# Performance work log

Hardware: AMD Instinct MI355X
Metric: run time of the kernel (lower is better)

## Reference

```python
import jax, jax.numpy as jnp
import numpy as np

B, S, D = 16, 4096, 64
N_HASHES, BUCKET_SIZE = 8, 64
TOKEN_SELF_ATTN_VALUE = -50000.0


def setup_inputs() -> dict:
    key = jax.random.key(0)
    k1, k2, k3 = jax.random.split(key, 3)
    qk = jax.random.normal(k1, (B, S, D), jnp.float32)
    v = jax.random.normal(k2, (B, S, D), jnp.float32)
    # random rotations for LSH hashing: (batch, dim, n_hashes, n_buckets//2)
    rotations = jax.random.normal(k3, (B, D, N_HASHES, (S // BUCKET_SIZE) // 2), jnp.float32)
    return {"qk": qk, "v": v, "rotations": rotations}


def _look_one_back(x):
    # concat each chunk with the previous chunk (wrapping): (b, c, n, ...) -> (b, c, 2n, ...)
    return jnp.concatenate([x, jnp.roll(x, 1, axis=1)], axis=2)


def _lsh_attention(qk, v, rotations):
    b, s, d = qk.shape
    n_buckets = s // BUCKET_SIZE
    # --- hash vectors (rehash_each_round=True path) ---
    rotated = jnp.einsum('btf,bfhi->bhti', qk, rotations)          # (b, h, s, nb/2)
    rotated = jnp.concatenate([rotated, -rotated], axis=-1)        # (b, h, s, nb)
    buckets = jnp.argmax(rotated, axis=-1)                          # (b, h, s)
    offsets = (jnp.arange(N_HASHES) * n_buckets)[None, :, None]
    buckets = (buckets + offsets).reshape(b, -1)                    # (b, h*s)
    # --- stable bucket sort of tokens ---
    ticker = jnp.arange(N_HASHES * s)[None, :]
    buckets_and_t = s * buckets + ticker % s
    sticker = jnp.argsort(buckets_and_t, axis=-1)                   # sorted order
    undo_sort = jnp.argsort(sticker, axis=-1)
    st = sticker % s                                                # original token index
    sqk = jnp.take_along_axis(qk, st[..., None], axis=1)            # (b, h*s, d)
    sv = jnp.take_along_axis(v, st[..., None], axis=1)
    chunk_size = N_HASHES * n_buckets
    bq_t = st.reshape(b, chunk_size, -1)                            # (b, c, n)
    bqk = sqk.reshape(b, chunk_size, -1, d)                         # (b, c, n, d)
    bv = sv.reshape(b, chunk_size, -1, d)
    # shared-QK: keys are L2-normalized queries
    norm = jnp.linalg.norm(bqk, axis=-1, keepdims=True)
    bk = bqk / jnp.maximum(norm, 1e-12)
    bk = _look_one_back(bk)                                         # (b, c, 2n, d)
    bvl = _look_one_back(bv)
    bkv_t = _look_one_back(bq_t)                                    # (b, c, 2n)
    dots = jnp.einsum('bhie,bhje->bhij', bqk, bk) * (d ** -0.5)     # (b, c, n, 2n)
    # mask self-attention (token attends to itself only as last resort)
    self_mask = bq_t[:, :, :, None] == bkv_t[:, :, None, :]
    dots = jnp.where(self_mask, TOKEN_SELF_ATTN_VALUE, dots)
    # stable softmax per chunk; keep logsumexp for cross-round combination
    lse = jax.nn.logsumexp(dots, axis=-1, keepdims=True)            # (b, c, n, 1)
    p = jnp.exp(dots - lse)
    bo = jnp.einsum('buij,buje->buie', p, bvl)                      # (b, c, n, d)
    so = bo.reshape(b, -1, d)                                       # (b, h*s, d)
    slogits = lse.reshape(b, -1)                                    # (b, h*s)
    # undo the sort
    o = jnp.take_along_axis(so, undo_sort[..., None], axis=1)
    logits = jnp.take_along_axis(slogits, undo_sort, axis=1)
    o = o.reshape(b, N_HASHES, s, d)
    logits = logits.reshape(b, N_HASHES, s, 1)
    # combine hash rounds weighted by softmax over per-round logsumexp
    probs = jnp.exp(logits - jax.nn.logsumexp(logits, axis=1, keepdims=True))
    return jnp.sum(o * probs, axis=1)                               # (b, s, d)


def reference(qk, v, rotations):
    return _lsh_attention(qk, v, rotations)
```

## Files before the change

kernel.cpp:

```cpp
#include <hip/hip_runtime.h>
#include <math.h>

#define NB_B 16
#define NB_S 4096
#define NB_D 64
#define NB_H 8

#define KSTR 72
#define PSTR 136
#define VSTR 72

typedef _Float16 half_t;
typedef __attribute__((ext_vector_type(2))) _Float16 half2t;
typedef __attribute__((ext_vector_type(4))) _Float16 half4;
typedef __attribute__((ext_vector_type(8))) _Float16 half8;
typedef __attribute__((ext_vector_type(4))) float floatx4;
typedef __attribute__((ext_vector_type(2))) float f32x2;

__global__ __launch_bounds__(256) void prep_kernel(const float* __restrict__ qk,
                                                   const float* __restrict__ v,
                                                   half_t* __restrict__ khat,
                                                   half_t* __restrict__ vh,
                                                   float* __restrict__ norm) {
  int g = blockIdx.x * 256 + threadIdx.x;
  float4 qv = ((const float4*)qk)[g];
  float4 vv = ((const float4*)v)[g];
  float ss = qv.x * qv.x + qv.y * qv.y + qv.z * qv.z + qv.w * qv.w;
  for (int off = 1; off < 16; off <<= 1) ss += __shfl_xor(ss, off);
  float nr = fmaxf(sqrtf(ss), 1e-12f);
  float sc = 1.0f / nr;
  half4 hk = {(half_t)(qv.x * sc), (half_t)(qv.y * sc), (half_t)(qv.z * sc),
              (half_t)(qv.w * sc)};
  half4 hv = {(half_t)vv.x, (half_t)vv.y, (half_t)vv.z, (half_t)vv.w};
  ((half4*)khat)[g] = hk;
  ((half4*)vh)[g] = hv;
  if ((threadIdx.x & 15) == 0) norm[g >> 4] = nr;
}

__global__ __launch_bounds__(256) void hash_kernel(const float* __restrict__ qk,
                                                   const float* __restrict__ rot,
                                                   int* __restrict__ bkt) {
  __shared__ float rotS[64 * 32];
  int tid = threadIdx.x;
  int blk = blockIdx.x;
  int tile = blk & 15, bh = blk >> 4;
  int h = bh & 7, b = bh >> 3;
  int t = (tile << 8) + tid;

  for (int i = tid; i < 2048; i += 256) {
    int f = i >> 5, ii = i & 31;
    rotS[i] = rot[(((size_t)b * 64 + f) * 8 + h) * 32 + ii];
  }
  __syncthreads();

  const float4* qrow = (const float4*)(qk + (((size_t)b << 12) + t) * 64);
  float qreg[64];
#pragma unroll
  for (int j = 0; j < 16; j++) *(float4*)(qreg + 4 * j) = qrow[j];

  f32x2 acc2[16];
#pragma unroll
  for (int i = 0; i < 16; i++) acc2[i] = (f32x2){0.f, 0.f};

  {
#pragma clang fp contract(off)
#pragma unroll
    for (int f = 0; f < 64; f++) {
      float qf = qreg[f];
      f32x2 q2 = {qf, qf};
      const f32x2* wrow = (const f32x2*)(rotS + f * 32);
#pragma unroll
      for (int i2 = 0; i2 < 16; i2++) {
        f32x2 prod = q2 * wrow[i2];
        acc2[i2] = acc2[i2] + prod;
      }
    }
  }

  float b1 = acc2[0][0];
  int i1 = 0;
#pragma unroll
  for (int i = 1; i < 32; i++) {
    float x = acc2[i >> 1][i & 1];
    if (x > b1) { b1 = x; i1 = i; }
  }
#pragma unroll
  for (int i = 0; i < 32; i++) {
    float x = -acc2[i >> 1][i & 1];
    if (x > b1) { b1 = x; i1 = 32 + i; }
  }
  bkt[(((size_t)(b * 8 + h)) << 12) + t] = i1;
}

__global__ __launch_bounds__(256) void sort_kernel(const int* __restrict__ bkt,
                                                   int* __restrict__ st) {
  __shared__ int lb[4096];
  __shared__ int hist[4096];
  __shared__ int cumoff[64];
  int tid = threadIdx.x;
  int b = blockIdx.x >> 3, h = blockIdx.x & 7;
  const int* gb = bkt + (((size_t)(b * 8 + h)) << 12);
  for (int t = tid; t < 4096; t += 256) lb[t] = gb[t];
  for (int i = tid; i < 4096; i += 256) hist[i] = 0;
  __syncthreads();
  for (int t = tid; t < 4096; t += 256) atomicAdd(&hist[((t >> 6) << 6) | lb[t]], 1);
  __syncthreads();
  if (tid < 64) {
    int run = 0;
    for (int cc = 0; cc < 64; cc++) {
      int x = hist[(cc << 6) | tid];
      hist[(cc << 6) | tid] = run;
      run += x;
    }
    int s = run;
    for (int off = 1; off < 64; off <<= 1) {
      int u = __shfl_up(s, off);
      if (tid >= off) s += u;
    }
    cumoff[tid] = s - run;
  }
  __syncthreads();
  int lane = tid & 63;
  for (int p = 0; p < 16; p++) {
    int t = (p << 8) + tid;
    int vb = lb[t];
    unsigned long long m = 0xFFFFFFFFFFFFFFFFull;
#pragma unroll
    for (int bit = 0; bit < 6; bit++) {
      unsigned long long bl = __ballot((vb >> bit) & 1);
      m &= ((vb >> bit) & 1) ? bl : ~bl;
    }
    int rank = __popcll(m & ((1ull << lane) - 1ull));
    int cpos = cumoff[vb] + hist[((t >> 6) << 6) | vb] + rank;
    st[(((size_t)(b * 8 + h)) << 12) + cpos] = t;
  }
}

__global__ __launch_bounds__(256) void chunk_kernel(const half_t* __restrict__ khat,
                                                    const half_t* __restrict__ vh,
                                                    const float* __restrict__ norm,
                                                    const int* __restrict__ st,
                                                    half_t* __restrict__ oh,
                                                    float* __restrict__ lse) {
  __shared__ __align__(16) half_t Ks[128 * KSTR];
  __shared__ __align__(16) half_t Vt[64 * VSTR];
  __shared__ int tk[128];
  __shared__ float normS[64];
  __shared__ float invS[64];
  int tid = threadIdx.x;
  int g = blockIdx.x & 511;
  int b = blockIdx.x >> 9;
  int h = g >> 6, c = g & 63;
  int gp = (g + 511) & 511;
  int hp = gp >> 6, cp = gp & 63;
  if (tid < 64) {
    tk[tid] = st[(((size_t)(b * 8 + h)) << 12) + (c << 6) + tid];
  } else if (tid < 128) {
    tk[tid] = st[(((size_t)(b * 8 + hp)) << 12) + (cp << 6) + (tid - 64)];
  }
  __syncthreads();
  if (tid < 64) normS[tid] = norm[(b << 12) + tk[tid]];
  for (int idx = tid; idx < 1024; idx += 256) {
    int row = idx >> 3, fo = idx & 7;
    half8 val = *(const half8*)(khat + (((size_t)(b << 12) + tk[row]) << 6) + fo * 8);
    *(half8*)(Ks + row * KSTR + fo * 8) = val;
  }
  {
    int kp = tid & 31, ch = tid >> 5;
    half8 r0 = *(const half8*)(vh + (((size_t)(b << 12) + tk[2 * kp]) << 6) + ch * 8);
    half8 r1 = *(const half8*)(vh + (((size_t)(b << 12) + tk[2 * kp + 1]) << 6) + ch * 8);
#pragma unroll
    for (int j = 0; j < 8; j++) {
      half2t pr = {r0[j], r1[j]};
      *(half2t*)(Vt + (ch * 8 + j) * VSTR + 2 * kp) = pr;
    }
  }
  __syncthreads();

  int lane = tid & 63, w = tid >> 6;
  int m = lane & 15, quad = lane >> 4;
  half8 afr[2];
#pragma unroll
  for (int ki = 0; ki < 2; ki++)
    afr[ki] = *(const half8*)(Ks + (w * 16 + m) * KSTR + ki * 32 + quad * 8);
  int ti[4];
  float scr[4];
#pragma unroll
  for (int r = 0; r < 4; r++) {
    int rr = w * 16 + quad * 4 + r;
    ti[r] = tk[rr];
    scr[r] = 0.125f * normS[rr];
  }

  float p[8][4];
#pragma unroll
  for (int nt = 0; nt < 8; nt++) {
    floatx4 acc = {0.f, 0.f, 0.f, 0.f};
#pragma unroll
    for (int ki = 0; ki < 2; ki++) {
      half8 bfr = *(const half8*)(Ks + (nt * 16 + m) * KSTR + ki * 32 + quad * 8);
      acc = __builtin_amdgcn_mfma_f32_16x16x32_f16(afr[ki], bfr, acc, 0, 0, 0);
    }
    int tj = tk[nt * 16 + m];
#pragma unroll
    for (int r = 0; r < 4; r++)
      p[nt][r] = (ti[r] == tj) ? 0.f : __expf(fmaf(acc[r], scr[r], -scr[r]));
  }

  float lr[4];
#pragma unroll
  for (int r = 0; r < 4; r++) {
    float ll = 0.f;
#pragma unroll
    for (int nt = 0; nt < 8; nt++) ll += p[nt][r];
    for (int off = 1; off < 16; off <<= 1) ll += __shfl_xor(ll, off);
    lr[r] = ll;
    if (m == 0) {
      lse[(((size_t)(b * 8 + h)) << 12) + ti[r]] = scr[r] + __logf(ll);
      invS[w * 16 + quad * 4 + r] = 1.0f / ll;
    }
  }
  __syncthreads();

  half_t* Ps = Ks;
#pragma unroll
  for (int nt = 0; nt < 8; nt++) {
#pragma unroll
    for (int r = 0; r < 4; r++) {
      Ps[(w * 16 + quad * 4 + r) * PSTR + nt * 16 + m] = (half_t)p[nt][r];
    }
  }
  __syncthreads();

  half8 pfr[4];
#pragma unroll
  for (int kk = 0; kk < 4; kk++)
    pfr[kk] = *(const half8*)(Ps + (w * 16 + m) * PSTR + kk * 32 + quad * 8);

  floatx4 accO[4];
#pragma unroll
  for (int dt = 0; dt < 4; dt++) accO[dt] = (floatx4){0.f, 0.f, 0.f, 0.f};

#pragma unroll
  for (int dt = 0; dt < 4; dt++) {
#pragma unroll
    for (int kk = 0; kk < 2; kk++) {
      half8 vfr = *(const half8*)(Vt + (dt * 16 + m) * VSTR + kk * 32 + quad * 8);
      accO[dt] = __builtin_amdgcn_mfma_f32_16x16x32_f16(vfr, pfr[kk], accO[dt], 0, 0, 0);
    }
  }
  __syncthreads();

  {
    int kp = tid & 31, ch = tid >> 5;
    half8 r0 = *(const half8*)(vh + (((size_t)(b << 12) + tk[64 + 2 * kp]) << 6) + ch * 8);
    half8 r1 = *(const half8*)(vh + (((size_t)(b << 12) + tk[65 + 2 * kp]) << 6) + ch * 8);
#pragma unroll
    for (int j = 0; j < 8; j++) {
      half2t pr = {r0[j], r1[j]};
      *(half2t*)(Vt + (ch * 8 + j) * VSTR + 2 * kp) = pr;
    }
  }
  __syncthreads();

#pragma unroll
  for (int dt = 0; dt < 4; dt++) {
#pragma unroll
    for (int kk = 2; kk < 4; kk++) {
      half8 vfr = *(const half8*)(Vt + (dt * 16 + m) * VSTR + (kk - 2) * 32 + quad * 8);
      accO[dt] = __builtin_amdgcn_mfma_f32_16x16x32_f16(vfr, pfr[kk], accO[dt], 0, 0, 0);
    }
  }

  {
    int tt = tk[w * 16 + m];
    float inv = invS[w * 16 + m];
    half_t* dst = oh + ((((size_t)(b * 8 + h)) << 12) + tt) * 64 + quad * 4;
#pragma unroll
    for (int dt = 0; dt < 4; dt++) {
      half4 ov = {(half_t)(accO[dt][0] * inv), (half_t)(accO[dt][1] * inv),
                  (half_t)(accO[dt][2] * inv), (half_t)(accO[dt][3] * inv)};
      *(half4*)(dst + dt * 16) = ov;
    }
  }
}

__global__ __launch_bounds__(256) void combine_kernel(const half_t* __restrict__ oh,
                                                      const float* __restrict__ lse,
                                                      float* __restrict__ out) {
  int idx = blockIdx.x * 256 + threadIdx.x;
  int do8 = idx & 7;
  int ts = idx >> 3;
  int b = ts >> 12, t = ts & 4095;
  size_t base = ((size_t)b << 15) + t;
  float L[8];
  float m = -3.4e38f;
#pragma unroll
  for (int h = 0; h < 8; h++) {
    L[h] = lse[base + ((size_t)h << 12)];
    m = fmaxf(m, L[h]);
  }
  float s = 0.f;
#pragma unroll
  for (int h = 0; h < 8; h++) s += __expf(L[h] - m);
  float lt = m + __logf(s);
  float acc[8];
#pragma unroll
  for (int j = 0; j < 8; j++) acc[j] = 0.f;
#pragma unroll
  for (int h = 0; h < 8; h++) {
    float wgt = __expf(L[h] - lt);
    half8 o = *(const half8*)(oh + ((base + ((size_t)h << 12)) << 6) + do8 * 8);
#pragma unroll
    for (int j = 0; j < 8; j++) acc[j] += wgt * (float)o[j];
  }
  float* dst = out + ((((size_t)b << 12) + t) << 6) + do8 * 8;
  *(float4*)dst = (float4){acc[0], acc[1], acc[2], acc[3]};
  *(float4*)(dst + 4) = (float4){acc[4], acc[5], acc[6], acc[7]};
}

extern "C" void kernel_launch(void* const* d_in, const int* in_sizes, int n_in,
                              void* d_out, int out_size, void* d_ws, size_t ws_size,
                              hipStream_t stream) {
  const float* qk = (const float*)d_in[0];
  const float* v = (const float*)d_in[1];
  const float* rot = (const float*)d_in[2];
  float* out = (float*)d_out;

  int* bkt = (int*)d_ws;
  int* stp = bkt + NB_B * NB_H * NB_S;
  float* lse = (float*)(stp + NB_B * NB_H * NB_S);
  float* norm = lse + NB_B * NB_H * NB_S;
  half_t* khat = (half_t*)(norm + NB_B * NB_S);
  half_t* vh = khat + (size_t)NB_B * NB_S * NB_D;
  half_t* oh = vh + (size_t)NB_B * NB_S * NB_D;

  prep_kernel<<<NB_B * NB_S * 16 / 256, 256, 0, stream>>>(qk, v, khat, vh, norm);
  hash_kernel<<<NB_B * NB_H * 16, 256, 0, stream>>>(qk, rot, bkt);
  sort_kernel<<<NB_B * NB_H, 256, 0, stream>>>(bkt, stp);
  chunk_kernel<<<NB_B * 512, 256, 0, stream>>>(khat, vh, norm, stp, oh, lse);
  combine_kernel<<<NB_B * NB_S * 8 / 256, 256, 0, stream>>>(oh, lse, out);
}
```

Before: 215.0 us.

## Compute LSH hash projections with fp16 MFMA and recompute near-ties in fp32

Replaces the scalar fp32 hash projection with an fp16 MFMA matrix multiply. Each token's argmax over the rotated values is found with a cross-lane shuffle reduction that also tracks the runner-up. Tokens whose top-two margin falls below a threshold go into a per-(batch,hash) list, and a fixup kernel recomputes their bucket in exact fp32 so the result matches the reference. This moves most of the hashing FLOPs onto matrix cores, at the cost of an extra memset, an extra kernel launch, atomics, and reliance on the margin threshold being large enough to cover fp16 error.

```diff
diff --git a/kernel.cpp b/kernel.cpp
--- a/kernel.cpp
+++ b/kernel.cpp
@@ -15,7 +15,6 @@
 typedef __attribute__((ext_vector_type(4))) _Float16 half4;
 typedef __attribute__((ext_vector_type(8))) _Float16 half8;
 typedef __attribute__((ext_vector_type(4))) float floatx4;
-typedef __attribute__((ext_vector_type(2))) float f32x2;
 
 __global__ __launch_bounds__(256) void prep_kernel(const float* __restrict__ qk,
                                                    const float* __restrict__ v,
@@ -37,59 +36,138 @@
   if ((threadIdx.x & 15) == 0) norm[g >> 4] = nr;
 }
 
-__global__ __launch_bounds__(256) void hash_kernel(const float* __restrict__ qk,
-                                                   const float* __restrict__ rot,
-                                                   int* __restrict__ bkt) {
+__global__ __launch_bounds__(256) void hash_mfma_kernel(const float* __restrict__ qk,
+                                                        const float* __restrict__ rot,
+                                                        int* __restrict__ bkt,
+                                                        int* __restrict__ cnt,
+                                                        int* __restrict__ list) {
+  __shared__ __align__(16) half_t Qh[128 * 72];
+  __shared__ __align__(16) half_t Rt[32 * 72];
+  int tid = threadIdx.x;
+  int blk = blockIdx.x;
+  int tile = blk & 31, bh = blk >> 5;
+  int h = bh & 7, b = bh >> 3;
+  int t0 = tile << 7;
+
+  for (int idx = tid; idx < 2048; idx += 256) {
+    int f = idx >> 5, i = idx & 31;
+    Rt[i * 72 + f] = (half_t)rot[(((size_t)b * 64 + f) * 8 + h) * 32 + i];
+  }
+  for (int idx = tid; idx < 1024; idx += 256) {
+    int row = idx >> 3, fo = idx & 7;
+    const float* src = qk + (((size_t)b << 12) + t0 + row) * 64 + fo * 8;
+    float4 a = *(const float4*)src;
+    float4 c = *(const float4*)(src + 4);
+    half8 hv = {(half_t)a.x, (half_t)a.y, (half_t)a.z, (half_t)a.w,
+                (half_t)c.x, (half_t)c.y, (half_t)c.z, (half_t)c.w};
+    *(half8*)(Qh + row * 72 + fo * 8) = hv;
+  }
+  __syncthreads();
+
+  int lane = tid & 63, w = tid >> 6;
+  int m = lane & 15, quad = lane >> 4;
+  half8 bfr[2][2];
+#pragma unroll
+  for (int nt = 0; nt < 2; nt++)
+#pragma unroll
+    for (int ki = 0; ki < 2; ki++)
+      bfr[nt][ki] = *(const half8*)(Rt + (nt * 16 + m) * 72 + ki * 32 + quad * 8);
+
+#pragma unroll
+  for (int mt8 = 0; mt8 < 2; mt8++) {
+    int mt = w + mt8 * 4;
+    half8 afr[2];
+#pragma unroll
+    for (int ki = 0; ki < 2; ki++)
+      afr[ki] = *(const half8*)(Qh + (mt * 16 + m) * 72 + ki * 32 + quad * 8);
+    floatx4 acc0 = {0.f, 0.f, 0.f, 0.f}, acc1 = {0.f, 0.f, 0.f, 0.f};
+#pragma unroll
+    for (int ki = 0; ki < 2; ki++) {
+      acc0 = __builtin_amdgcn_mfma_f32_16x16x32_f16(afr[ki], bfr[0][ki], acc0, 0, 0, 0);
+      acc1 = __builtin_amdgcn_mfma_f32_16x16x32_f16(afr[ki], bfr[1][ki], acc1, 0, 0, 0);
+    }
+#pragma unroll
+    for (int r = 0; r < 4; r++) {
+      float a0 = acc0[r], a1 = acc1[r];
+      float v1 = a0, v2;
+      int i1 = m;
+      if (a1 > v1) { v2 = v1; v1 = a1; i1 = 16 + m; } else v2 = a1;
+      float na0 = -a0;
+      if (na0 > v1) { v2 = v1; v1 = na0; i1 = 32 + m; } else if (na0 > v2) v2 = na0;
+      float na1 = -a1;
+      if (na1 > v1) { v2 = v1; v1 = na1; i1 = 48 + m; } else if (na1 > v2) v2 = na1;
+#pragma unroll
+      for (int off = 1; off < 16; off <<= 1) {
+        float ov1 = __shfl_xor(v1, off);
+        int oi1 = __shfl_xor(i1, off);
+        float ov2 = __shfl_xor(v2, off);
+        bool take = (ov1 > v1) || (ov1 == v1 && oi1 < i1);
+        float nv2 = take ? fmaxf(ov2, v1) : fmaxf(v2, ov1);
+        v1 = take ? ov1 : v1;
+        i1 = take ? oi1 : i1;
+        v2 = nv2;
+      }
+      if (m == 0) {
+        int token = t0 + mt * 16 + quad * 4 + r;
+        bkt[((size_t)bh << 12) + token] = i1;
+        if (v1 - v2 < 0.0625f) {
+          int pos = atomicAdd(&cnt[bh], 1);
+          list[(bh << 12) + (pos & 4095)] = token;
+        }
+      }
+    }
+  }
+}
+
+__global__ __launch_bounds__(256) void hash_fixup_kernel(const float* __restrict__ qk,
+                                                         const float* __restrict__ rot,
+                                                         const int* __restrict__ cnt,
+                                                         const int* __restrict__ list,
+                                                         int* __restrict__ bkt) {
   __shared__ float rotS[64 * 32];
   int tid = threadIdx.x;
-  int blk = blockIdx.x;
-  int tile = blk & 15, bh = blk >> 4;
+  int bh = blockIdx.x;
   int h = bh & 7, b = bh >> 3;
-  int t = (tile << 8) + tid;
-
   for (int i = tid; i < 2048; i += 256) {
     int f = i >> 5, ii = i & 31;
     rotS[i] = rot[(((size_t)b * 64 + f) * 8 + h) * 32 + ii];
   }
   __syncthreads();
-
-  const float4* qrow = (const float4*)(qk + (((size_t)b << 12) + t) * 64);
-  float qreg[64];
-#pragma unroll
-  for (int j = 0; j < 16; j++) *(float4*)(qreg + 4 * j) = qrow[j];
-
-  f32x2 acc2[16];
-#pragma unroll
-  for (int i = 0; i < 16; i++) acc2[i] = (f32x2){0.f, 0.f};
-
-  {
-#pragma clang fp contract(off)
+  int n = cnt[bh];
+  if (n > 4096) n = 4096;
+  for (int j = tid; j < n; j += 256) {
+    int t = list[(bh << 12) + j];
+    const float4* qrow = (const float4*)(qk + (((size_t)b << 12) + t) * 64);
+    float qreg[64];
+#pragma unroll
+    for (int jj = 0; jj < 16; jj++) *(float4*)(qreg + 4 * jj) = qrow[jj];
+    float acc[32];
+#pragma unroll
+    for (int i = 0; i < 32; i++) acc[i] = 0.f;
 #pragma unroll
     for (int f = 0; f < 64; f++) {
       float qf = qreg[f];
-      f32x2 q2 = {qf, qf};
-      const f32x2* wrow = (const f32x2*)(rotS + f * 32);
-#pragma unroll
-      for (int i2 = 0; i2 < 16; i2++) {
-        f32x2 prod = q2 * wrow[i2];
-        acc2[i2] = acc2[i2] + prod;
+#pragma unroll
+      for (int i4 = 0; i4 < 8; i4++) {
+        float4 wv = *(const float4*)(rotS + f * 32 + i4 * 4);
+        acc[i4 * 4 + 0] = __fadd_rn(acc[i4 * 4 + 0], __fmul_rn(qf, wv.x));
+        acc[i4 * 4 + 1] = __fadd_rn(acc[i4 * 4 + 1], __fmul_rn(qf, wv.y));
+        acc[i4 * 4 + 2] = __fadd_rn(acc[i4 * 4 + 2], __fmul_rn(qf, wv.z));
+        acc[i4 * 4 + 3] = __fadd_rn(acc[i4 * 4 + 3], __fmul_rn(qf, wv.w));
       }
     }
-  }
-
-  float b1 = acc2[0][0];
-  int i1 = 0;
-#pragma unroll
-  for (int i = 1; i < 32; i++) {
-    float x = acc2[i >> 1][i & 1];
-    if (x > b1) { b1 = x; i1 = i; }
-  }
-#pragma unroll
-  for (int i = 0; i < 32; i++) {
-    float x = -acc2[i >> 1][i & 1];
-    if (x > b1) { b1 = x; i1 = 32 + i; }
-  }
-  bkt[(((size_t)(b * 8 + h)) << 12) + t] = i1;
+    float b1 = acc[0];
+    int i1 = 0;
+#pragma unroll
+    for (int i = 1; i < 32; i++)
+      if (acc[i] > b1) { b1 = acc[i]; i1 = i; }
+#pragma unroll
+    for (int i = 0; i < 32; i++) {
+      float x = -acc[i];
+      if (x > b1) { b1 = x; i1 = 32 + i; }
+    }
+    bkt[((size_t)bh << 12) + t] = i1;
+  }
 }
 
 __global__ __launch_bounds__(256) void sort_kernel(const int* __restrict__ bkt,
@@ -334,9 +412,13 @@
   half_t* khat = (half_t*)(norm + NB_B * NB_S);
   half_t* vh = khat + (size_t)NB_B * NB_S * NB_D;
   half_t* oh = vh + (size_t)NB_B * NB_S * NB_D;
-
+  int* cnt = (int*)(oh + (size_t)NB_B * NB_H * NB_S * NB_D);
+  int* list = cnt + 128;
+
+  hipMemsetAsync(cnt, 0, 128 * sizeof(int), stream);
   prep_kernel<<<NB_B * NB_S * 16 / 256, 256, 0, stream>>>(qk, v, khat, vh, norm);
-  hash_kernel<<<NB_B * NB_H * 16, 256, 0, stream>>>(qk, rot, bkt);
+  hash_mfma_kernel<<<NB_B * NB_H * 32, 256, 0, stream>>>(qk, rot, bkt, cnt, list);
+  hash_fixup_kernel<<<NB_B * NB_H, 256, 0, stream>>>(qk, rot, cnt, list, bkt);
   sort_kernel<<<NB_B * NB_H, 256, 0, stream>>>(bkt, stp);
   chunk_kernel<<<NB_B * 512, 256, 0, stream>>>(khat, vh, norm, stp, oh, lse);
   combine_kernel<<<NB_B * NB_S * 8 / 256, 256, 0, stream>>>(oh, lse, out);
```

Measured after the change: 247.1 us. 1.15x slower.
